# Kernel optimization log

Hardware: AMD Instinct MI355X
Metric: run time of the kernel (lower is better)

Reference implementation:

```python
import jax, jax.numpy as jnp
import numpy as np

H_DIM = 64      # input_dim of edge_aggregation (== h_dim)
HID = 128       # hidden_size of each per-edge-type agg MLP
T = 5           # edge_types for non-nba dataset
B, E, N = 64, 1024, 512


def setup_inputs() -> dict:
    key = jax.random.key(0)
    ks = jax.random.split(key, 8)
    edge_distribution = jax.random.uniform(ks[0], (B, E, T), dtype=jnp.float32)
    H = jax.random.uniform(ks[1], (B, E, N), dtype=jnp.float32)
    ori = jax.random.normal(ks[2], (B, N, H_DIM), dtype=jnp.float32)
    s1 = 1.0 / np.sqrt(H_DIM)
    s2 = 1.0 / np.sqrt(HID)
    # stacked per-edge-type MLP params: Linear(64->128) -> ReLU -> Linear(128->64)
    W1 = jax.random.uniform(ks[3], (T, H_DIM, HID), minval=-s1, maxval=s1, dtype=jnp.float32)
    b1 = jax.random.uniform(ks[4], (T, HID), minval=-s1, maxval=s1, dtype=jnp.float32)
    W2 = jax.random.uniform(ks[5], (T, HID, H_DIM), minval=-s2, maxval=s2, dtype=jnp.float32)
    b2 = jax.random.uniform(ks[6], (T, H_DIM), minval=-s2, maxval=s2, dtype=jnp.float32)
    return {"edge_distribution": edge_distribution, "H": H, "ori": ori,
            "W1": W1, "b1": b1, "W2": W2, "b2": b2}


def reference(edge_distribution, H, ori, W1, b1, W2, b2):
    # incidence gather: hyperedge features [B, E, D]
    edges = jnp.matmul(H, ori)
    # per-edge-type 2-layer MLP, vectorized over the T edge types
    h = jax.nn.relu(jnp.einsum('bed,tdh->bteh', edges, W1) + b1[None, :, None, :])
    per_type = jnp.einsum('bteh,thd->bted', h, W2) + b2[None, :, None, :]
    # mixture-weighted sum over edge types -> [B, E, D]
    edge_feature = jnp.einsum('bet,bted->bed', edge_distribution, per_type)
    # scatter back through H^T and concat with original node features
    node_agg = jnp.einsum('ben,bed->bnd', H, edge_feature)  # H^T @ edge_feature
    node_feature = jnp.concatenate((node_agg, ori), axis=-1)  # [B, N, 2D]
    return node_feature
```

## Files before the change

kernel.cpp:

```cpp
#include <hip/hip_runtime.h>

#define B_   64
#define E_   1024
#define N_   512
#define D_   64
#define HID_ 128
#define T_   5

typedef __bf16 bf16x8 __attribute__((ext_vector_type(8)));
typedef float f32x4 __attribute__((ext_vector_type(4)));

__device__ __forceinline__ unsigned short f2bu(float f) {
    union { float f; unsigned int u; } v; v.f = f;
    unsigned int r = (v.u + 0x7fffu + ((v.u >> 16) & 1u)) >> 16;
    return (unsigned short)r;
}

__device__ __forceinline__ unsigned int pack2(float lo, float hi) {
    union { __bf16 b[2]; unsigned int u; } v;
    v.b[0] = (__bf16)lo; v.b[1] = (__bf16)hi;
    return v.u;
}

__device__ __forceinline__ uint4 cvt8(float4 a, float4 b) {
    union { __bf16 h[8]; uint4 u; } v;
    v.h[0] = (__bf16)a.x; v.h[1] = (__bf16)a.y; v.h[2] = (__bf16)a.z; v.h[3] = (__bf16)a.w;
    v.h[4] = (__bf16)b.x; v.h[5] = (__bf16)b.y; v.h[6] = (__bf16)b.z; v.h[7] = (__bf16)b.w;
    return v.u;
}

#define MFMA16(a, b, c) __builtin_amdgcn_mfma_f32_16x16x32_bf16((a), (b), (c), 0, 0, 0)

__global__ __launch_bounds__(256) void k_prep_w(const float* __restrict__ W1,
                                                const float* __restrict__ W2,
                                                unsigned short* __restrict__ W1T,
                                                unsigned short* __restrict__ W2T) {
    int idx = blockIdx.x * 256 + threadIdx.x;
    if (idx < T_ * HID_ * D_) {
        int t = idx / (HID_ * D_), rem = idx % (HID_ * D_);
        int h = rem / D_, d = rem % D_;
        W1T[idx] = f2bu(W1[(t * D_ + d) * HID_ + h]);
    } else {
        int j = idx - T_ * HID_ * D_;
        int t = j / (D_ * HID_), rem = j % (D_ * HID_);
        int d = rem / HID_, h = rem % HID_;
        W2T[j] = f2bu(W2[(t * HID_ + h) * D_ + d]);
    }
}

__global__ __launch_bounds__(256) void k_ori_prep(const float* __restrict__ ori,
                                                  float* __restrict__ out,
                                                  unsigned short* __restrict__ oriT) {
    int b = blockIdx.y, n0 = blockIdx.x * 64;
    __shared__ float tl[64 * 65];
    int tid = threadIdx.x;
    int dl = tid & 63;
    #pragma unroll 4
    for (int p = 0; p < 16; ++p) {
        int nn = p * 4 + (tid >> 6);
        float v = ori[(size_t)(b * N_ + n0 + nn) * D_ + dl];
        out[(size_t)(b * N_ + n0 + nn) * 128 + 64 + dl] = v;
        tl[dl * 65 + nn] = v;
    }
    __syncthreads();
    #pragma unroll 4
    for (int p = 0; p < 16; ++p) {
        int dd = p * 4 + (tid >> 6);
        oriT[(size_t)(b * D_ + dd) * N_ + n0 + dl] = f2bu(tl[dd * 65 + dl]);
    }
}

__global__ __launch_bounds__(256) void k_edge_mlp(const float* __restrict__ H,
                                                  const unsigned short* __restrict__ oriT,
                                                  const float* __restrict__ ed,
                                                  const float* __restrict__ b1,
                                                  const float* __restrict__ b2,
                                                  const unsigned short* __restrict__ W1T,
                                                  const unsigned short* __restrict__ W2T,
                                                  unsigned short* __restrict__ efT) {
    int bx = blockIdx.x;
    int b = bx >> 4, e0 = (bx & 15) * 64;
    __shared__ __align__(16) unsigned short aA[64 * 72];
    __shared__ __align__(16) unsigned short bB[64 * 72];
    __shared__ __align__(16) unsigned short a_sh[64 * 72];
    __shared__ __align__(16) unsigned short w_sh[128 * 72];
    __shared__ __align__(16) unsigned short h_sh[64 * 136];
    __shared__ float wd_sh[320];
    __shared__ float b1_sh[640];
    __shared__ float b2_sh[320];
    int tid = threadIdx.x, w = tid >> 6, l = tid & 63, q = l >> 4, c = l & 15;

    for (int u = tid; u < 320; u += 256) wd_sh[u] = ed[((size_t)b * E_ + e0) * T_ + u];
    for (int u = tid; u < 640; u += 256) b1_sh[u] = b1[u];
    for (int u = tid; u < 320; u += 256) b2_sh[u] = b2[u];

    const f32x4 zero = {0.f, 0.f, 0.f, 0.f};

    f32x4 acc1[4];
    #pragma unroll
    for (int fn = 0; fn < 4; ++fn) acc1[fn] = zero;

    for (int ks = 0; ks < 8; ++ks) {
        int k0 = ks * 64;
        #pragma unroll
        for (int p = 0; p < 2; ++p) {
            int u = p * 256 + tid, r = u >> 3, sg = u & 7;
            const float* s = &H[((size_t)b * E_ + e0 + r) * N_ + k0 + sg * 8];
            float4 f0 = *(const float4*)&s[0];
            float4 f1 = *(const float4*)&s[4];
            *(uint4*)&aA[r * 72 + sg * 8] = cvt8(f0, f1);
        }
        #pragma unroll
        for (int p = 0; p < 2; ++p) {
            int u = p * 256 + tid, r = u >> 3, sg = u & 7;
            *(uint4*)&bB[r * 72 + sg * 8] =
                *(const uint4*)&oriT[((size_t)b * D_ + r) * N_ + k0 + sg * 8];
        }
        __syncthreads();
        #pragma unroll
        for (int h = 0; h < 2; ++h) {
            bf16x8 a0 = *(const bf16x8*)&aA[(w * 16 + c) * 72 + h * 32 + q * 8];
            #pragma unroll
            for (int fn = 0; fn < 4; ++fn) {
                bf16x8 bb = *(const bf16x8*)&bB[(fn * 16 + c) * 72 + h * 32 + q * 8];
                acc1[fn] = MFMA16(a0, bb, acc1[fn]);
            }
        }
        __syncthreads();
    }
    #pragma unroll
    for (int fn = 0; fn < 4; ++fn)
        #pragma unroll
        for (int i = 0; i < 4; ++i)
            a_sh[(w * 16 + q * 4 + i) * 72 + fn * 16 + c] = f2bu(acc1[fn][i]);

    f32x4 y[4];
    #pragma unroll
    for (int fn = 0; fn < 4; ++fn) y[fn] = zero;

    for (int t = 0; t < T_; ++t) {
        __syncthreads();
        #pragma unroll
        for (int p = 0; p < 4; ++p) {
            int u = p * 256 + tid, hh = u >> 3, sg = u & 7;
            *(uint4*)&w_sh[hh * 72 + sg * 8] =
                *(const uint4*)&W1T[(t * HID_ + hh) * D_ + sg * 8];
        }
        __syncthreads();
        f32x4 hc[8];
        #pragma unroll
        for (int fn = 0; fn < 8; ++fn) hc[fn] = zero;
        #pragma unroll
        for (int ks = 0; ks < 2; ++ks) {
            bf16x8 a = *(const bf16x8*)&a_sh[(w * 16 + c) * 72 + ks * 32 + q * 8];
            #pragma unroll
            for (int fn = 0; fn < 8; ++fn) {
                bf16x8 bb = *(const bf16x8*)&w_sh[(fn * 16 + c) * 72 + ks * 32 + q * 8];
                hc[fn] = MFMA16(a, bb, hc[fn]);
            }
        }
        float wv[4];
        #pragma unroll
        for (int i = 0; i < 4; ++i) wv[i] = wd_sh[(w * 16 + q * 4 + i) * T_ + t];
        #pragma unroll
        for (int fn = 0; fn < 8; ++fn) {
            float b1v = b1_sh[t * HID_ + fn * 16 + c];
            #pragma unroll
            for (int i = 0; i < 4; ++i) {
                float v = hc[fn][i] + b1v;
                v = fmaxf(v, 0.0f) * wv[i];
                h_sh[(w * 16 + q * 4 + i) * 136 + fn * 16 + c] = f2bu(v);
            }
        }
        __syncthreads();
        #pragma unroll
        for (int p = 0; p < 4; ++p) {
            int u = p * 256 + tid, dd = u >> 4, sg = u & 15;
            *(uint4*)&w_sh[dd * 136 + sg * 8] =
                *(const uint4*)&W2T[(t * D_ + dd) * HID_ + sg * 8];
        }
        __syncthreads();
        #pragma unroll
        for (int ks = 0; ks < 4; ++ks) {
            bf16x8 a = *(const bf16x8*)&h_sh[(w * 16 + c) * 136 + ks * 32 + q * 8];
            #pragma unroll
            for (int fn = 0; fn < 4; ++fn) {
                bf16x8 bb = *(const bf16x8*)&w_sh[(fn * 16 + c) * 136 + ks * 32 + q * 8];
                y[fn] = MFMA16(a, bb, y[fn]);
            }
        }
    }
    #pragma unroll
    for (int fn = 0; fn < 4; ++fn) {
        int d = fn * 16 + c;
        ushort4 o;
        #pragma unroll
        for (int i = 0; i < 4; ++i) {
            int r = w * 16 + q * 4 + i;
            float s = y[fn][i];
            #pragma unroll
            for (int t = 0; t < T_; ++t) s += wd_sh[r * T_ + t] * b2_sh[t * D_ + d];
            ((unsigned short*)&o)[i] = f2bu(s);
        }
        *(ushort4*)&efT[((size_t)b * D_ + d) * E_ + e0 + w * 16 + q * 4] = o;
    }
}

__global__ __launch_bounds__(256) void k_gemm_out(const float* __restrict__ H,
                                                  const unsigned short* __restrict__ efT,
                                                  float* __restrict__ out) {
    int b = blockIdx.y, n0 = blockIdx.x * 64;
    __shared__ __align__(16) unsigned short aA[64 * 72];
    __shared__ unsigned int bB32[64 * 33];
    int tid = threadIdx.x, w = tid >> 6, l = tid & 63, q = l >> 4, c = l & 15;
    int r2 = tid >> 3, cg = tid & 7;
    const f32x4 zero = {0.f, 0.f, 0.f, 0.f};
    f32x4 acc[4];
    #pragma unroll
    for (int fm = 0; fm < 4; ++fm) acc[fm] = zero;

    for (int ks = 0; ks < 16; ++ks) {
        int k0 = ks * 64;
        #pragma unroll
        for (int p = 0; p < 2; ++p) {
            int u = p * 256 + tid, r = u >> 3, sg = u & 7;
            *(uint4*)&aA[r * 72 + sg * 8] =
                *(const uint4*)&efT[((size_t)b * D_ + r) * E_ + k0 + sg * 8];
        }
        {
            const float* s0 = &H[((size_t)b * E_ + k0 + 2 * r2) * N_ + n0 + cg * 8];
            const float* s1 = s0 + N_;
            float4 f0 = *(const float4*)&s0[0], f1 = *(const float4*)&s0[4];
            float4 g0 = *(const float4*)&s1[0], g1 = *(const float4*)&s1[4];
            float r0[8] = {f0.x, f0.y, f0.z, f0.w, f1.x, f1.y, f1.z, f1.w};
            float r1[8] = {g0.x, g0.y, g0.z, g0.w, g1.x, g1.y, g1.z, g1.w};
            #pragma unroll
            for (int j = 0; j < 8; ++j)
                bB32[(cg * 8 + j) * 33 + r2] = pack2(r0[j], r1[j]);
        }
        __syncthreads();
        #pragma unroll
        for (int h = 0; h < 2; ++h) {
            union { unsigned int u[4]; bf16x8 v; } bb;
            #pragma unroll
            for (int i = 0; i < 4; ++i)
                bb.u[i] = bB32[(w * 16 + c) * 33 + h * 16 + q * 4 + i];
            #pragma unroll
            for (int fm = 0; fm < 4; ++fm) {
                bf16x8 afr = *(const bf16x8*)&aA[(fm * 16 + c) * 72 + h * 32 + q * 8];
                acc[fm] = MFMA16(afr, bb.v, acc[fm]);
            }
        }
        __syncthreads();
    }
    #pragma unroll
    for (int fm = 0; fm < 4; ++fm) {
        *(f32x4*)&out[((size_t)b * N_ + n0 + w * 16 + c) * 128 + fm * 16 + q * 4] = acc[fm];
    }
}

extern "C" void kernel_launch(void* const* d_in, const int* in_sizes, int n_in,
                              void* d_out, int out_size, void* d_ws, size_t ws_size,
                              hipStream_t stream) {
    const float* ed  = (const float*)d_in[0];
    const float* H   = (const float*)d_in[1];
    const float* ori = (const float*)d_in[2];
    const float* W1  = (const float*)d_in[3];
    const float* b1  = (const float*)d_in[4];
    const float* W2  = (const float*)d_in[5];
    const float* b2  = (const float*)d_in[6];
    float* out = (float*)d_out;

    char* ws = (char*)d_ws;
    unsigned short* oriT = (unsigned short*)ws; ws += (size_t)B_ * D_ * N_ * 2;
    unsigned short* W1T  = (unsigned short*)ws; ws += (size_t)T_ * HID_ * D_ * 2;
    unsigned short* W2T  = (unsigned short*)ws; ws += (size_t)T_ * D_ * HID_ * 2;
    unsigned short* efT  = (unsigned short*)ws; ws += (size_t)B_ * D_ * E_ * 2;

    hipLaunchKernelGGL(k_prep_w, dim3(320), dim3(256), 0, stream, W1, W2, W1T, W2T);
    hipLaunchKernelGGL(k_ori_prep, dim3(8, 64), dim3(256), 0, stream, ori, out, oriT);
    hipLaunchKernelGGL(k_edge_mlp, dim3(1024), dim3(256), 0, stream,
                       H, oriT, ed, b1, b2, W1T, W2T, efT);
    hipLaunchKernelGGL(k_gemm_out, dim3(8, 64), dim3(256), 0, stream, H, efT, out);
}
```

Baseline: 276.8 us.

## Register-prefetch next tiles in both kernels and alias shared memory buffers

Both the edge-MLP kernel and the output GEMM now load the next K-tile of H, oriT and efT into registers while MFMAs run on the current tile in shared memory. The per-type W1/W2 weight loads are prefetched the same way. In the edge kernel the separate shared arrays are folded into one aliased buffer, which lowers LDS use and may allow more blocks per CU. The cost is higher register pressure, which could reduce occupancy.

```diff
diff --git a/kernel.cpp b/kernel.cpp
--- a/kernel.cpp
+++ b/kernel.cpp
@@ -80,15 +80,19 @@
                                                   unsigned short* __restrict__ efT) {
     int bx = blockIdx.x;
     int b = bx >> 4, e0 = (bx & 15) * 64;
-    __shared__ __align__(16) unsigned short aA[64 * 72];
-    __shared__ __align__(16) unsigned short bB[64 * 72];
-    __shared__ __align__(16) unsigned short a_sh[64 * 72];
-    __shared__ __align__(16) unsigned short w_sh[128 * 72];
-    __shared__ __align__(16) unsigned short h_sh[64 * 136];
+    __shared__ __align__(16) unsigned short lds[22528];
+    unsigned short* w_sh = lds;
+    unsigned short* a_sh = lds + 9216;
+    unsigned short* h_sh = lds + 13824;
     __shared__ float wd_sh[320];
     __shared__ float b1_sh[640];
     __shared__ float b2_sh[320];
     int tid = threadIdx.x, w = tid >> 6, l = tid & 63, q = l >> 4, c = l & 15;
+    int rA = tid >> 3, sgA = tid & 7;
+    int rA2 = tid >> 4, sgA2 = tid & 15;
+
+    unsigned short* aA = w_sh;
+    unsigned short* bB = w_sh + 4608;
 
     for (int u = tid; u < 320; u += 256) wd_sh[u] = ed[((size_t)b * E_ + e0) * T_ + u];
     for (int u = tid; u < 640; u += 256) b1_sh[u] = b1[u];
@@ -96,27 +100,42 @@
 
     const f32x4 zero = {0.f, 0.f, 0.f, 0.f};
 
+    uint4 w1r[4];
+    #pragma unroll
+    for (int p = 0; p < 4; ++p)
+        w1r[p] = *(const uint4*)&W1T[(size_t)(0 * HID_ + p * 32 + rA) * D_ + sgA * 8];
+
+    float4 hA0[2], hA1[2];
+    uint4 oB[2];
+    #pragma unroll
+    for (int p = 0; p < 2; ++p) {
+        const float* s = &H[((size_t)b * E_ + e0 + p * 32 + rA) * N_ + sgA * 8];
+        hA0[p] = *(const float4*)&s[0];
+        hA1[p] = *(const float4*)&s[4];
+        oB[p] = *(const uint4*)&oriT[((size_t)b * D_ + p * 32 + rA) * N_ + sgA * 8];
+    }
+
     f32x4 acc1[4];
     #pragma unroll
     for (int fn = 0; fn < 4; ++fn) acc1[fn] = zero;
 
     for (int ks = 0; ks < 8; ++ks) {
-        int k0 = ks * 64;
         #pragma unroll
         for (int p = 0; p < 2; ++p) {
-            int u = p * 256 + tid, r = u >> 3, sg = u & 7;
-            const float* s = &H[((size_t)b * E_ + e0 + r) * N_ + k0 + sg * 8];
-            float4 f0 = *(const float4*)&s[0];
-            float4 f1 = *(const float4*)&s[4];
-            *(uint4*)&aA[r * 72 + sg * 8] = cvt8(f0, f1);
-        }
-        #pragma unroll
-        for (int p = 0; p < 2; ++p) {
-            int u = p * 256 + tid, r = u >> 3, sg = u & 7;
-            *(uint4*)&bB[r * 72 + sg * 8] =
-                *(const uint4*)&oriT[((size_t)b * D_ + r) * N_ + k0 + sg * 8];
-        }
-        __syncthreads();
+            *(uint4*)&aA[(p * 32 + rA) * 72 + sgA * 8] = cvt8(hA0[p], hA1[p]);
+            *(uint4*)&bB[(p * 32 + rA) * 72 + sgA * 8] = oB[p];
+        }
+        __syncthreads();
+        if (ks < 7) {
+            int k0 = (ks + 1) * 64;
+            #pragma unroll
+            for (int p = 0; p < 2; ++p) {
+                const float* s = &H[((size_t)b * E_ + e0 + p * 32 + rA) * N_ + k0 + sgA * 8];
+                hA0[p] = *(const float4*)&s[0];
+                hA1[p] = *(const float4*)&s[4];
+                oB[p] = *(const uint4*)&oriT[((size_t)b * D_ + p * 32 + rA) * N_ + k0 + sgA * 8];
+            }
+        }
         #pragma unroll
         for (int h = 0; h < 2; ++h) {
             bf16x8 a0 = *(const bf16x8*)&aA[(w * 16 + c) * 72 + h * 32 + q * 8];
@@ -141,11 +160,12 @@
     for (int t = 0; t < T_; ++t) {
         __syncthreads();
         #pragma unroll
-        for (int p = 0; p < 4; ++p) {
-            int u = p * 256 + tid, hh = u >> 3, sg = u & 7;
-            *(uint4*)&w_sh[hh * 72 + sg * 8] =
-                *(const uint4*)&W1T[(t * HID_ + hh) * D_ + sg * 8];
-        }
+        for (int p = 0; p < 4; ++p)
+            *(uint4*)&w_sh[(p * 32 + rA) * 72 + sgA * 8] = w1r[p];
+        uint4 w2r[4];
+        #pragma unroll
+        for (int p = 0; p < 4; ++p)
+            w2r[p] = *(const uint4*)&W2T[(size_t)(t * D_ + p * 16 + rA2) * HID_ + sgA2 * 8];
         __syncthreads();
         f32x4 hc[8];
         #pragma unroll
@@ -174,10 +194,12 @@
         }
         __syncthreads();
         #pragma unroll
-        for (int p = 0; p < 4; ++p) {
-            int u = p * 256 + tid, dd = u >> 4, sg = u & 15;
-            *(uint4*)&w_sh[dd * 136 + sg * 8] =
-                *(const uint4*)&W2T[(t * D_ + dd) * HID_ + sg * 8];
+        for (int p = 0; p < 4; ++p)
+            *(uint4*)&w_sh[(p * 16 + rA2) * 136 + sgA2 * 8] = w2r[p];
+        if (t < 4) {
+            #pragma unroll
+            for (int p = 0; p < 4; ++p)
+                w1r[p] = *(const uint4*)&W1T[(size_t)((t + 1) * HID_ + p * 32 + rA) * D_ + sgA * 8];
         }
         __syncthreads();
         #pragma unroll
@@ -219,26 +241,40 @@
     #pragma unroll
     for (int fm = 0; fm < 4; ++fm) acc[fm] = zero;
 
+    uint4 aR[2];
+    float4 f0, f1, g0, g1;
+    #pragma unroll
+    for (int p = 0; p < 2; ++p)
+        aR[p] = *(const uint4*)&efT[((size_t)b * D_ + p * 32 + r2) * E_ + cg * 8];
+    {
+        const float* s0 = &H[((size_t)b * E_ + 2 * r2) * N_ + n0 + cg * 8];
+        const float* s1 = s0 + N_;
+        f0 = *(const float4*)&s0[0]; f1 = *(const float4*)&s0[4];
+        g0 = *(const float4*)&s1[0]; g1 = *(const float4*)&s1[4];
+    }
+
     for (int ks = 0; ks < 16; ++ks) {
-        int k0 = ks * 64;
-        #pragma unroll
-        for (int p = 0; p < 2; ++p) {
-            int u = p * 256 + tid, r = u >> 3, sg = u & 7;
-            *(uint4*)&aA[r * 72 + sg * 8] =
-                *(const uint4*)&efT[((size_t)b * D_ + r) * E_ + k0 + sg * 8];
-        }
+        #pragma unroll
+        for (int p = 0; p < 2; ++p)
+            *(uint4*)&aA[(p * 32 + r2) * 72 + cg * 8] = aR[p];
         {
+            float r0[8] = {f0.x, f0.y, f0.z, f0.w, f1.x, f1.y, f1.z, f1.w};
+            float r1[8] = {g0.x, g0.y, g0.z, g0.w, g1.x, g1.y, g1.z, g1.w};
+            #pragma unroll
+            for (int j = 0; j < 8; ++j)
+                bB32[(cg * 8 + j) * 33 + r2] = pack2(r0[j], r1[j]);
+        }
+        __syncthreads();
+        if (ks < 15) {
+            int k0 = (ks + 1) * 64;
+            #pragma unroll
+            for (int p = 0; p < 2; ++p)
+                aR[p] = *(const uint4*)&efT[((size_t)b * D_ + p * 32 + r2) * E_ + k0 + cg * 8];
             const float* s0 = &H[((size_t)b * E_ + k0 + 2 * r2) * N_ + n0 + cg * 8];
             const float* s1 = s0 + N_;
-            float4 f0 = *(const float4*)&s0[0], f1 = *(const float4*)&s0[4];
-            float4 g0 = *(const float4*)&s1[0], g1 = *(const float4*)&s1[4];
-            float r0[8] = {f0.x, f0.y, f0.z, f0.w, f1.x, f1.y, f1.z, f1.w};
-            float r1[8] = {g0.x, g0.y, g0.z, g0.w, g1.x, g1.y, g1.z, g1.w};
-            #pragma unroll
-            for (int j = 0; j < 8; ++j)
-                bB32[(cg * 8 + j) * 33 + r2] = pack2(r0[j], r1[j]);
-        }
-        __syncthreads();
+            f0 = *(const float4*)&s0[0]; f1 = *(const float4*)&s0[4];
+            g0 = *(const float4*)&s1[0]; g1 = *(const float4*)&s1[4];
+        }
         #pragma unroll
         for (int h = 0; h < 2; ++h) {
             union { unsigned int u[4]; bf16x8 v; } bb;
```

Measured after the change: 347.5 us. 1.26x slower.
